# Performance work log

Hardware: AMD Instinct MI355X
Metric: run time of the kernel (lower is better)

## Reference

```python
import jax, jax.numpy as jnp
import numpy as np

IN_C, OUT_C = 64, 128
HID = OUT_C // 4  # 32
NEG = 0.1  # LeakyReLU slope inside MLPs


def _leaky(x, slope):
    return jnp.where(x >= 0, x, slope * x)


def gather_neighbors(x, idx):
    # x: [B,N,F], idx: [B,N',K] -> [B,N',K,F]
    return jax.vmap(lambda xb, ib: xb[ib])(x, idx)


def setup_inputs() -> dict:
    key = jax.random.key(0)
    ks = jax.random.split(key, 12)
    B, N, K = 2, 65536, 16
    x = jax.random.normal(ks[0], (B, N, IN_C), dtype=jnp.float32)
    pos = jax.random.uniform(ks[1], (B, N, 3), dtype=jnp.float32)
    neighbor_idx = jax.random.randint(ks[2], (B, N, K), 0, N)
    s = lambda fi, fo: 1.0 / np.sqrt(fi)
    W_in = jax.random.normal(ks[3], (IN_C, HID), dtype=jnp.float32) * s(IN_C, HID)
    b_in = jnp.zeros((HID,), jnp.float32)
    Wa = jax.random.normal(ks[4], (3, HID), dtype=jnp.float32) * s(3, HID)
    ba = jnp.zeros((HID,), jnp.float32)
    Wb = jax.random.normal(ks[5], (HID, HID), dtype=jnp.float32) * s(HID, HID)
    bb = jnp.zeros((HID,), jnp.float32)
    W_out = jax.random.normal(ks[6], (HID, OUT_C), dtype=jnp.float32) * s(HID, OUT_C)
    b_out = jnp.zeros((OUT_C,), jnp.float32)
    W_sc = jax.random.normal(ks[7], (IN_C, OUT_C), dtype=jnp.float32) * s(IN_C, OUT_C)
    b_sc = jnp.zeros((OUT_C,), jnp.float32)
    return dict(x=x, pos=pos, neighbor_idx=neighbor_idx,
                W_in=W_in, b_in=b_in, Wa=Wa, ba=ba, Wb=Wb, bb=bb,
                W_out=W_out, b_out=b_out, W_sc=W_sc, b_sc=b_sc)


def reference(x, pos, neighbor_idx, W_in, b_in, Wa, ba, Wb, bb, W_out, b_out, W_sc, b_sc):
    # shortcut (in_channels != out_channels -> Linear)
    residual = x @ W_sc + b_sc                      # [B,N,OUT]
    h = _leaky(x @ W_in + b_in, NEG)                # [B,N,HID]
    # PointConv: per-edge weights from relative positions
    nbr_pos = gather_neighbors(pos, neighbor_idx)   # [B,N,K,3]
    rel = pos[:, :, None, :] - nbr_pos              # [B,N,K,3]
    w = _leaky(rel @ Wa + ba, NEG) @ Wb + bb        # [B,N,K,HID]
    hg = gather_neighbors(h, neighbor_idx)          # [B,N,K,HID]
    conv = jnp.sum(w * hg, axis=2)                  # [B,N,HID]
    out = conv @ W_out + b_out                      # [B,N,OUT]
    return _leaky(out + residual, 0.01)             # F.leaky_relu default slope
```

## Files before the change

### kernel.cpp

```cpp
#include <hip/hip_runtime.h>
#include <hip/hip_bf16.h>

#define IN_C 64
#define OUT_C 128
#define HID 32
#define KNB 16

typedef __attribute__((ext_vector_type(8))) short short8;
typedef __attribute__((ext_vector_type(4))) float f32x4;

__device__ __forceinline__ float leaky(float v, float s) { return fmaxf(v, s * v); }

__device__ __forceinline__ unsigned bf16u(float f) {
    __hip_bfloat16 h = __float2bfloat16(f);
    return (unsigned)*reinterpret_cast<unsigned short*>(&h);
}
__device__ __forceinline__ short bf16s(float f) {
    __hip_bfloat16 h = __float2bfloat16(f);
    return *reinterpret_cast<short*>(&h);
}

__global__ __launch_bounds__(256) void pack_kernel(
    const float* __restrict__ pos, const float* __restrict__ Wout,
    const float* __restrict__ Wsc, float4* __restrict__ pos4,
    short* __restrict__ pk, int P)
{
    int t = blockIdx.x * 256 + threadIdx.x;
    if (t < 1536) {
        int ks = t >> 9, rem = t & 511;
        int nt = rem >> 6, g = (rem >> 4) & 3, n = rem & 15;
        int col = nt * 16 + n;
        short8 v;
        #pragma unroll
        for (int e = 0; e < 8; ++e) {
            int row = ks * 32 + 8 * g + e;
            float f = (row < 32) ? Wout[row * OUT_C + col]
                                 : Wsc[(row - 32) * OUT_C + col];
            v[e] = bf16s(f);
        }
        *(short8*)(pk + (long)t * 8) = v;
    }
    if (t < P) {
        float4 v;
        v.x = pos[3L * t + 0]; v.y = pos[3L * t + 1];
        v.z = pos[3L * t + 2]; v.w = 0.f;
        pos4[t] = v;
    }
}

__global__ __launch_bounds__(256) void hid_mfma(
    const float* __restrict__ x, const float* __restrict__ Win,
    const float* __restrict__ bin, unsigned* __restrict__ h2, int P)
{
    int lane = threadIdx.x & 63;
    int widx = __builtin_amdgcn_readfirstlane(threadIdx.x >> 6);
    int wavebase = (blockIdx.x * 4 + widx) * 16;
    if (wavebase >= P) return;
    int n = lane & 15, g = lane >> 4;

    short8 bfr[2][2];
    #pragma unroll
    for (int ks = 0; ks < 2; ++ks)
        #pragma unroll
        for (int nt = 0; nt < 2; ++nt)
            #pragma unroll
            for (int e = 0; e < 8; ++e)
                bfr[ks][nt][e] = bf16s(Win[(ks * 32 + 8 * g + e) * HID + nt * 16 + n]);

    float bv0 = bin[n], bv1 = bin[16 + n];

    const float* xr = x + (long)(wavebase + n) * IN_C;
    short8 a[2];
    #pragma unroll
    for (int ks = 0; ks < 2; ++ks) {
        float4 v0 = *(const float4*)(xr + ks * 32 + 8 * g);
        float4 v1 = *(const float4*)(xr + ks * 32 + 8 * g + 4);
        a[ks][0] = bf16s(v0.x); a[ks][1] = bf16s(v0.y);
        a[ks][2] = bf16s(v0.z); a[ks][3] = bf16s(v0.w);
        a[ks][4] = bf16s(v1.x); a[ks][5] = bf16s(v1.y);
        a[ks][6] = bf16s(v1.z); a[ks][7] = bf16s(v1.w);
    }

    f32x4 acc0 = { bv0, bv0, bv0, bv0 };
    f32x4 acc1 = { bv1, bv1, bv1, bv1 };
    acc0 = __builtin_amdgcn_mfma_f32_16x16x32_bf16(a[0], bfr[0][0], acc0, 0, 0, 0);
    acc0 = __builtin_amdgcn_mfma_f32_16x16x32_bf16(a[1], bfr[1][0], acc0, 0, 0, 0);
    acc1 = __builtin_amdgcn_mfma_f32_16x16x32_bf16(a[0], bfr[0][1], acc1, 0, 0, 0);
    acc1 = __builtin_amdgcn_mfma_f32_16x16x32_bf16(a[1], bfr[1][1], acc1, 0, 0, 0);

    #pragma unroll
    for (int r = 0; r < 4; ++r) {
        unsigned lo = bf16u(leaky(acc0[r], 0.1f));
        unsigned hi = bf16u(leaky(acc1[r], 0.1f));
        h2[(long)(wavebase + 4 * g + r) * 16 + n] = (hi << 16) | lo;
    }
}

__global__ __launch_bounds__(256) void edgeout_mfma(
    const float* __restrict__ x, const float4* __restrict__ pos4,
    const int* __restrict__ nbr, const unsigned* __restrict__ h2,
    const float* __restrict__ Wa, const float* __restrict__ ba,
    const float* __restrict__ Wb, const float* __restrict__ bb,
    const short* __restrict__ pk, const float* __restrict__ bout,
    const float* __restrict__ bsc, float* __restrict__ out, int N, int P)
{
    __shared__ float cbuf[4][32 * 17];

    int tid = threadIdx.x;
    int lane = tid & 63;
    int widx = __builtin_amdgcn_readfirstlane(tid >> 6);
    int n = lane & 15, g = lane >> 4;
    int wavebase = (blockIdx.x * 4 + widx) * 16;
    if (wavebase >= P) return;

    float waX[8], waY[8], waZ[8], bav[8];
    #pragma unroll
    for (int e = 0; e < 8; ++e) {
        int k = 8 * g + e;
        waX[e] = Wa[k]; waY[e] = Wa[HID + k]; waZ[e] = Wa[2 * HID + k];
        bav[e] = ba[k];
    }
    short8 wb0, wb1;
    #pragma unroll
    for (int e = 0; e < 8; ++e) {
        int k = 8 * g + e;
        wb0[e] = bf16s(Wb[k * HID + n]);
        wb1[e] = bf16s(Wb[k * HID + 16 + n]);
    }
    float bb0 = bb[n], bb1 = bb[16 + n];
    float* cb = cbuf[widx];

    #pragma unroll 1
    for (int pt = 0; pt < 16; ++pt) {
        int p = wavebase + pt;
        long pbase = (p >= N) ? (long)N : 0;
        float4 pp = pos4[p];

        const int* nrow = nbr + (long)p * KNB;
        long qt = pbase + nrow[n];
        float4 pq = pos4[qt];
        float rx = pp.x - pq.x, ry = pp.y - pq.y, rz = pp.z - pq.z;

        long q0 = pbase + nrow[4 * g + 0];
        long q1 = pbase + nrow[4 * g + 1];
        long q2 = pbase + nrow[4 * g + 2];
        long q3 = pbase + nrow[4 * g + 3];
        unsigned v0 = h2[q0 * 16 + n];
        unsigned v1 = h2[q1 * 16 + n];
        unsigned v2 = h2[q2 * 16 + n];
        unsigned v3 = h2[q3 * 16 + n];

        short8 af;
        #pragma unroll
        for (int e = 0; e < 8; ++e) {
            float tv = fmaf(rx, waX[e], fmaf(ry, waY[e], fmaf(rz, waZ[e], bav[e])));
            af[e] = bf16s(leaky(tv, 0.1f));
        }

        f32x4 w0 = { bb0, bb0, bb0, bb0 };
        f32x4 w1 = { bb1, bb1, bb1, bb1 };
        w0 = __builtin_amdgcn_mfma_f32_16x16x32_bf16(af, wb0, w0, 0, 0, 0);
        w1 = __builtin_amdgcn_mfma_f32_16x16x32_bf16(af, wb1, w1, 0, 0, 0);

        float hA0 = __uint_as_float(v0 << 16), hB0 = __uint_as_float(v0 & 0xffff0000u);
        float hA1 = __uint_as_float(v1 << 16), hB1 = __uint_as_float(v1 & 0xffff0000u);
        float hA2 = __uint_as_float(v2 << 16), hB2 = __uint_as_float(v2 & 0xffff0000u);
        float hA3 = __uint_as_float(v3 << 16), hB3 = __uint_as_float(v3 & 0xffff0000u);

        float pa = w0[0] * hA0 + w0[1] * hA1 + w0[2] * hA2 + w0[3] * hA3;
        float pb = w1[0] * hB0 + w1[1] * hB1 + w1[2] * hB2 + w1[3] * hB3;
        pa += __shfl_xor(pa, 16, 64);  pa += __shfl_xor(pa, 32, 64);
        pb += __shfl_xor(pb, 16, 64);  pb += __shfl_xor(pb, 32, 64);

        if (lane < 16) {
            cb[lane * 17 + pt]        = pa;
            cb[(lane + 16) * 17 + pt] = pb;
        }
    }
    asm volatile("s_waitcnt lgkmcnt(0)" ::: "memory");

    short8 a0, a1, a2;
    #pragma unroll
    for (int e = 0; e < 8; ++e)
        a0[e] = bf16s(cb[(8 * g + e) * 17 + n]);
    {
        const float* xr = x + (long)(wavebase + n) * IN_C;
        float4 u0 = *(const float4*)(xr + 8 * g);
        float4 u1 = *(const float4*)(xr + 8 * g + 4);
        float4 u2 = *(const float4*)(xr + 32 + 8 * g);
        float4 u3 = *(const float4*)(xr + 32 + 8 * g + 4);
        a1[0] = bf16s(u0.x); a1[1] = bf16s(u0.y); a1[2] = bf16s(u0.z); a1[3] = bf16s(u0.w);
        a1[4] = bf16s(u1.x); a1[5] = bf16s(u1.y); a1[6] = bf16s(u1.z); a1[7] = bf16s(u1.w);
        a2[0] = bf16s(u2.x); a2[1] = bf16s(u2.y); a2[2] = bf16s(u2.z); a2[3] = bf16s(u2.w);
        a2[4] = bf16s(u3.x); a2[5] = bf16s(u3.y); a2[6] = bf16s(u3.z); a2[7] = bf16s(u3.w);
    }

    #pragma unroll 1
    for (int nt = 0; nt < 8; ++nt) {
        short8 b0 = *(const short8*)(pk + ((long)(0 * 8 + nt) * 64 + lane) * 8);
        short8 b1 = *(const short8*)(pk + ((long)(1 * 8 + nt) * 64 + lane) * 8);
        short8 b2 = *(const short8*)(pk + ((long)(2 * 8 + nt) * 64 + lane) * 8);
        int o = nt * 16 + n;
        float bv = bout[o] + bsc[o];
        f32x4 acc = { bv, bv, bv, bv };
        acc = __builtin_amdgcn_mfma_f32_16x16x32_bf16(a0, b0, acc, 0, 0, 0);
        acc = __builtin_amdgcn_mfma_f32_16x16x32_bf16(a1, b1, acc, 0, 0, 0);
        acc = __builtin_amdgcn_mfma_f32_16x16x32_bf16(a2, b2, acc, 0, 0, 0);
        #pragma unroll
        for (int r = 0; r < 4; ++r)
            out[(long)(wavebase + 4 * g + r) * OUT_C + o] = leaky(acc[r], 0.01f);
    }
}

extern "C" void kernel_launch(void* const* d_in, const int* in_sizes, int n_in,
                              void* d_out, int out_size, void* d_ws, size_t ws_size,
                              hipStream_t stream) {
    const float* x    = (const float*)d_in[0];
    const float* pos  = (const float*)d_in[1];
    const int*   nbr  = (const int*)d_in[2];
    const float* Win  = (const float*)d_in[3];
    const float* bin  = (const float*)d_in[4];
    const float* Wa   = (const float*)d_in[5];
    const float* ba   = (const float*)d_in[6];
    const float* Wb   = (const float*)d_in[7];
    const float* bb   = (const float*)d_in[8];
    const float* Wout = (const float*)d_in[9];
    const float* bout = (const float*)d_in[10];
    const float* Wsc  = (const float*)d_in[11];
    const float* bsc  = (const float*)d_in[12];
    float* out = (float*)d_out;

    int P = in_sizes[0] / IN_C;
    int N = P / 2;

    unsigned* h2  = (unsigned*)d_ws;
    float4*  pos4 = (float4*)((char*)d_ws + (size_t)P * 64);
    short*   pk   = (short*)((char*)d_ws + (size_t)P * 64 + (size_t)P * 16);

    pack_kernel<<<(P + 255) / 256, 256, 0, stream>>>(pos, Wout, Wsc, pos4, pk, P);
    int blocks = (P + 63) / 64;
    hid_mfma<<<blocks, 256, 0, stream>>>(x, Win, bin, h2, P);
    edgeout_mfma<<<blocks, 256, 0, stream>>>(
        x, pos4, nbr, h2, Wa, ba, Wb, bb, pk, bout, bsc, out, N, P);
}
```

Baseline: 74.68 us.

## Software-pipeline neighbor gathers and shrink edgeout blocks to two waves

The edge kernel's 16-point loop is now fully unrolled. Neighbor indices are prefetched two points ahead and the pos/h gathers one point ahead, so global-load latency overlaps with the MFMA and reduction work. The x row loads are hoisted to kernel start, pbase is computed once per wave, and the output loop is unrolled by two. Blocks shrink to 128 threads with a waves-per-EU hint. This trades higher register pressure from the prefetch arrays for latency hiding, and may lower occupancy or cause spills.

```diff
diff --git a/kernel.cpp b/kernel.cpp
--- a/kernel.cpp
+++ b/kernel.cpp
@@ -96,7 +96,8 @@
     }
 }
 
-__global__ __launch_bounds__(256) void edgeout_mfma(
+__global__ __launch_bounds__(128) __attribute__((amdgpu_waves_per_eu(3, 4)))
+void edgeout_mfma(
     const float* __restrict__ x, const float4* __restrict__ pos4,
     const int* __restrict__ nbr, const unsigned* __restrict__ h2,
     const float* __restrict__ Wa, const float* __restrict__ ba,
@@ -104,14 +105,15 @@
     const short* __restrict__ pk, const float* __restrict__ bout,
     const float* __restrict__ bsc, float* __restrict__ out, int N, int P)
 {
-    __shared__ float cbuf[4][32 * 17];
+    __shared__ float cbuf[2][32 * 17];
 
     int tid = threadIdx.x;
     int lane = tid & 63;
     int widx = __builtin_amdgcn_readfirstlane(tid >> 6);
     int n = lane & 15, g = lane >> 4;
-    int wavebase = (blockIdx.x * 4 + widx) * 16;
+    int wavebase = (blockIdx.x * 2 + widx) * 16;
     if (wavebase >= P) return;
+    long pbase = (wavebase >= N) ? (long)N : 0;
 
     float waX[8], waY[8], waZ[8], bav[8];
     #pragma unroll
@@ -130,25 +132,37 @@
     float bb0 = bb[n], bb1 = bb[16 + n];
     float* cb = cbuf[widx];
 
-    #pragma unroll 1
-    for (int pt = 0; pt < 16; ++pt) {
-        int p = wavebase + pt;
-        long pbase = (p >= N) ? (long)N : 0;
-        float4 pp = pos4[p];
-
-        const int* nrow = nbr + (long)p * KNB;
-        long qt = pbase + nrow[n];
-        float4 pq = pos4[qt];
-        float rx = pp.x - pq.x, ry = pp.y - pq.y, rz = pp.z - pq.z;
-
-        long q0 = pbase + nrow[4 * g + 0];
-        long q1 = pbase + nrow[4 * g + 1];
-        long q2 = pbase + nrow[4 * g + 2];
-        long q3 = pbase + nrow[4 * g + 3];
-        unsigned v0 = h2[q0 * 16 + n];
-        unsigned v1 = h2[q1 * 16 + n];
-        unsigned v2 = h2[q2 * 16 + n];
-        unsigned v3 = h2[q3 * 16 + n];
+    const float* xr = x + (long)(wavebase + n) * IN_C;
+    float4 u0 = *(const float4*)(xr + 8 * g);
+    float4 u1 = *(const float4*)(xr + 8 * g + 4);
+    float4 u2 = *(const float4*)(xr + 32 + 8 * g);
+    float4 u3 = *(const float4*)(xr + 32 + 8 * g + 4);
+
+    int4  qv[KNB]; int qs[KNB];
+    float4 pp[KNB], pq[KNB];
+    unsigned hv[KNB][4];
+
+#define IDX(i) {                                                        \
+        const int* nr = nbr + (long)(wavebase + (i)) * KNB;             \
+        qv[i] = *(const int4*)(nr + 4 * g);                             \
+        qs[i] = nr[n]; }
+#define GATHER(i) {                                                     \
+        pp[i] = pos4[wavebase + (i)];                                   \
+        pq[i] = pos4[pbase + qs[i]];                                    \
+        hv[i][0] = h2[(pbase + qv[i].x) * 16 + n];                      \
+        hv[i][1] = h2[(pbase + qv[i].y) * 16 + n];                      \
+        hv[i][2] = h2[(pbase + qv[i].z) * 16 + n];                      \
+        hv[i][3] = h2[(pbase + qv[i].w) * 16 + n]; }
+
+    #pragma unroll
+    for (int pt = 0; pt < KNB; ++pt) {
+        if (pt == 0) { IDX(0) IDX(1) GATHER(0) }
+        if (pt + 2 < KNB) IDX(pt + 2)
+        if (pt + 1 < KNB) GATHER(pt + 1)
+
+        float rx = pp[pt].x - pq[pt].x;
+        float ry = pp[pt].y - pq[pt].y;
+        float rz = pp[pt].z - pq[pt].z;
 
         short8 af;
         #pragma unroll
@@ -162,40 +176,34 @@
         w0 = __builtin_amdgcn_mfma_f32_16x16x32_bf16(af, wb0, w0, 0, 0, 0);
         w1 = __builtin_amdgcn_mfma_f32_16x16x32_bf16(af, wb1, w1, 0, 0, 0);
 
-        float hA0 = __uint_as_float(v0 << 16), hB0 = __uint_as_float(v0 & 0xffff0000u);
-        float hA1 = __uint_as_float(v1 << 16), hB1 = __uint_as_float(v1 & 0xffff0000u);
-        float hA2 = __uint_as_float(v2 << 16), hB2 = __uint_as_float(v2 & 0xffff0000u);
-        float hA3 = __uint_as_float(v3 << 16), hB3 = __uint_as_float(v3 & 0xffff0000u);
-
-        float pa = w0[0] * hA0 + w0[1] * hA1 + w0[2] * hA2 + w0[3] * hA3;
-        float pb = w1[0] * hB0 + w1[1] * hB1 + w1[2] * hB2 + w1[3] * hB3;
+        float hA0 = __uint_as_float(hv[pt][0] << 16), hB0 = __uint_as_float(hv[pt][0] & 0xffff0000u);
+        float hA1 = __uint_as_float(hv[pt][1] << 16), hB1 = __uint_as_float(hv[pt][1] & 0xffff0000u);
+        float hA2 = __uint_as_float(hv[pt][2] << 16), hB2 = __uint_as_float(hv[pt][2] & 0xffff0000u);
+        float hA3 = __uint_as_float(hv[pt][3] << 16), hB3 = __uint_as_float(hv[pt][3] & 0xffff0000u);
+
+        float pa = fmaf(w0[0], hA0, fmaf(w0[1], hA1, fmaf(w0[2], hA2, w0[3] * hA3)));
+        float pb = fmaf(w1[0], hB0, fmaf(w1[1], hB1, fmaf(w1[2], hB2, w1[3] * hB3)));
         pa += __shfl_xor(pa, 16, 64);  pa += __shfl_xor(pa, 32, 64);
         pb += __shfl_xor(pb, 16, 64);  pb += __shfl_xor(pb, 32, 64);
 
-        if (lane < 16) {
-            cb[lane * 17 + pt]        = pa;
-            cb[(lane + 16) * 17 + pt] = pb;
-        }
-    }
+        if (g == 0)      cb[n * 17 + pt]        = pa;
+        else if (g == 1) cb[(n + 16) * 17 + pt] = pb;
+    }
+#undef IDX
+#undef GATHER
+
     asm volatile("s_waitcnt lgkmcnt(0)" ::: "memory");
 
     short8 a0, a1, a2;
     #pragma unroll
     for (int e = 0; e < 8; ++e)
         a0[e] = bf16s(cb[(8 * g + e) * 17 + n]);
-    {
-        const float* xr = x + (long)(wavebase + n) * IN_C;
-        float4 u0 = *(const float4*)(xr + 8 * g);
-        float4 u1 = *(const float4*)(xr + 8 * g + 4);
-        float4 u2 = *(const float4*)(xr + 32 + 8 * g);
-        float4 u3 = *(const float4*)(xr + 32 + 8 * g + 4);
-        a1[0] = bf16s(u0.x); a1[1] = bf16s(u0.y); a1[2] = bf16s(u0.z); a1[3] = bf16s(u0.w);
-        a1[4] = bf16s(u1.x); a1[5] = bf16s(u1.y); a1[6] = bf16s(u1.z); a1[7] = bf16s(u1.w);
-        a2[0] = bf16s(u2.x); a2[1] = bf16s(u2.y); a2[2] = bf16s(u2.z); a2[3] = bf16s(u2.w);
-        a2[4] = bf16s(u3.x); a2[5] = bf16s(u3.y); a2[6] = bf16s(u3.z); a2[7] = bf16s(u3.w);
-    }
-
-    #pragma unroll 1
+    a1[0] = bf16s(u0.x); a1[1] = bf16s(u0.y); a1[2] = bf16s(u0.z); a1[3] = bf16s(u0.w);
+    a1[4] = bf16s(u1.x); a1[5] = bf16s(u1.y); a1[6] = bf16s(u1.z); a1[7] = bf16s(u1.w);
+    a2[0] = bf16s(u2.x); a2[1] = bf16s(u2.y); a2[2] = bf16s(u2.z); a2[3] = bf16s(u2.w);
+    a2[4] = bf16s(u3.x); a2[5] = bf16s(u3.y); a2[6] = bf16s(u3.z); a2[7] = bf16s(u3.w);
+
+    #pragma unroll 2
     for (int nt = 0; nt < 8; ++nt) {
         short8 b0 = *(const short8*)(pk + ((long)(0 * 8 + nt) * 64 + lane) * 8);
         short8 b1 = *(const short8*)(pk + ((long)(1 * 8 + nt) * 64 + lane) * 8);
@@ -238,8 +246,7 @@
     short*   pk   = (short*)((char*)d_ws + (size_t)P * 64 + (size_t)P * 16);
 
     pack_kernel<<<(P + 255) / 256, 256, 0, stream>>>(pos, Wout, Wsc, pos4, pk, P);
-    int blocks = (P + 63) / 64;
-    hid_mfma<<<blocks, 256, 0, stream>>>(x, Win, bin, h2, P);
-    edgeout_mfma<<<blocks, 256, 0, stream>>>(
+    hid_mfma<<<(P + 63) / 64, 256, 0, stream>>>(x, Win, bin, h2, P);
+    edgeout_mfma<<<(P + 31) / 32, 128, 0, stream>>>(
         x, pos4, nbr, h2, Wa, ba, Wb, bb, pk, bout, bsc, out, N, P);
 }
```

After: 67.28 us. 9.9% less time.
